# Performance work log

Hardware: AMD Instinct MI355X
Metric: run time of the kernel (lower is better)

## Reference

```python
import jax, jax.numpy as jnp
import numpy as np

B, NQ, DM = 2, 8192, 256
NH, DH, NL, NP = 6, 64, 3, 9
IMG_H, IMG_W = 384, 1280
SHAPES = [(48, 160), (24, 80), (12, 40)]  # (h, w) per pyramid level


def setup_inputs() -> dict:
    key = jax.random.key(0)
    ks = jax.random.split(key, 16)
    inp = {}
    inp["x"] = jax.random.normal(ks[0], (B, NQ, DM), jnp.float32)
    inp["pe"] = jax.random.normal(ks[1], (B, NQ, DM), jnp.float32)
    # lidar points in front of the camera so projected uv mostly lands in-image
    u = jax.random.uniform(ks[2], (B, NQ, 3), jnp.float32)
    inp["coor"] = jnp.stack([(u[..., 0] - 0.5) * 40.0,
                             (u[..., 1] - 0.5) * 4.0,
                             2.0 + u[..., 2] * 48.0], axis=-1)
    K = jnp.array([[700., 0., 640., 0.], [0., 700., 192., 0.],
                   [0., 0., 1., 0.], [0., 0., 0., 1.]], jnp.float32)
    inp["cam2img"] = jnp.broadcast_to(K, (B, 4, 4))
    inp["lidar2cam"] = jnp.broadcast_to(jnp.eye(4, dtype=jnp.float32), (B, 4, 4))
    for i, (h, w) in enumerate(SHAPES):
        inp[f"feat{i}"] = jax.random.normal(ks[3 + i], (B, DM, h, w), jnp.float32) * 0.1
    s = 1.0 / np.sqrt(DM).astype(np.float32)
    inp["W_value"] = jax.random.normal(ks[6], (DM, NH * DH), jnp.float32) * s
    inp["b_value"] = jnp.zeros((NH * DH,), jnp.float32)
    inp["W_off"] = jax.random.normal(ks[7], (DM, NH * NL * NP * 2), jnp.float32) * 0.01
    inp["b_off"] = jax.random.normal(ks[8], (NH * NL * NP * 2,), jnp.float32)
    inp["W_attn"] = jax.random.normal(ks[9], (DM, NH * NL * NP), jnp.float32) * s
    inp["b_attn"] = jnp.zeros((NH * NL * NP,), jnp.float32)
    inp["W_out"] = jax.random.normal(ks[10], (NH * DH, DM), jnp.float32) * (1.0 / np.sqrt(NH * DH)).astype(np.float32)
    inp["b_out"] = jnp.zeros((DM,), jnp.float32)
    return inp


def _points2uv(points, cam2img, lidar2cam):
    R, t = lidar2cam[:, :3, :3], lidar2cam[:, :3, 3]
    pc = jnp.einsum('bij,bnj->bni', R, points) + t[:, None, :]
    Kr, Kt = cam2img[:, :3, :3], cam2img[:, :3, 3]
    p2 = jnp.einsum('bij,bnj->bni', Kr, pc) + Kt[:, None, :]
    return p2[..., :2] / p2[..., 2:3]  # [B,NQ,2] (u,v)


def _bilinear_gather(v, loc, hl, wl):
    # v: [B*NH, hl*wl, DH] values; loc: [B,NQ,NH,NP,2] normalized [0,1]
    # matches grid_sample(bilinear, padding=zeros, align_corners=False)
    x = loc[..., 0] * wl - 0.5
    y = loc[..., 1] * hl - 0.5
    x0 = jnp.floor(x)
    y0 = jnp.floor(y)
    fx = x - x0
    fy = y - y0
    acc = jnp.zeros((B, NH, NQ, NP, DH), v.dtype)
    for dy in (0, 1):
        for dx in (0, 1):
            xi = x0 + dx
            yi = y0 + dy
            wgt = (fx if dx else 1.0 - fx) * (fy if dy else 1.0 - fy)
            valid = (xi >= 0) & (xi < wl) & (yi >= 0) & (yi < hl)
            idx = (jnp.clip(yi, 0, hl - 1) * wl + jnp.clip(xi, 0, wl - 1)).astype(jnp.int32)
            idx = idx.transpose(0, 2, 1, 3).reshape(B * NH, NQ * NP)
            g = jax.vmap(lambda vt, it: vt[it])(v, idx)  # [B*NH, NQ*NP, DH]
            g = g.reshape(B, NH, NQ, NP, DH)
            wv = (wgt * valid).transpose(0, 2, 1, 3)      # [B,NH,NQ,NP]
            acc = acc + g * wv[..., None]
    return acc


def reference(x, pe, coor, cam2img, lidar2cam, feat0, feat1, feat2,
              W_value, b_value, W_off, b_off, W_attn, b_attn, W_out, b_out):
    feats = [feat0, feat1, feat2]
    uv = _points2uv(coor, cam2img, lidar2cam)  # [B,NQ,2]
    # per-level reference points in level pixel coords: uv * (w_l/W, h_l/H)
    ref = jnp.stack([uv * jnp.array([w / IMG_W, h / IMG_H], jnp.float32)
                     for (h, w) in SHAPES], axis=2)  # [B,NQ,NL,2]
    q = x + pe
    off = (q @ W_off + b_off).reshape(B, NQ, NH, NL, NP, 2)
    attn = jax.nn.softmax((q @ W_attn + b_attn).reshape(B, NQ, NH, NL * NP), axis=-1)
    attn = attn.reshape(B, NQ, NH, NL, NP).transpose(0, 2, 1, 3, 4)  # [B,NH,NQ,NL,NP]
    norm = jnp.array([[w, h] for (h, w) in SHAPES], jnp.float32)     # [NL,2] (w,h)
    loc = (ref[:, :, None, :, None, :] + off) / norm[None, None, None, :, None, :]
    out = jnp.zeros((B, NH, NQ, DH), jnp.float32)
    for l, (h, w) in enumerate(SHAPES):
        src = feats[l].reshape(B, DM, h * w).transpose(0, 2, 1)  # [B,hw,DM]
        v = (src @ W_value + b_value).reshape(B, h * w, NH, DH)
        v = v.transpose(0, 2, 1, 3).reshape(B * NH, h * w, DH)
        sampled = _bilinear_gather(v, loc[:, :, :, l], h, w)    # [B,NH,NQ,NP,DH]
        out = out + jnp.einsum('bhqp,bhqpd->bhqd', attn[:, :, :, l], sampled)
    out = out.transpose(0, 2, 1, 3).reshape(B, NQ, NH * DH)
    return out @ W_out + b_out  # dropout is identity at eval
```

## Files before the change

### kernel.cpp

```cpp
#include <hip/hip_runtime.h>
#include <hip/hip_bf16.h>

#define NQ_   8192
#define DM_   256
#define NH_   6
#define DH_   64
#define BATCH 2

typedef __attribute__((ext_vector_type(8))) short short8;
typedef __attribute__((ext_vector_type(4))) short short4v;
typedef __attribute__((ext_vector_type(4))) float float4v;
typedef __attribute__((ext_vector_type(2))) float f32x2;
typedef __attribute__((ext_vector_type(4))) unsigned int uint32x4;
typedef __attribute__((ext_vector_type(4))) int int32x4;

#if defined(__has_builtin)
#if __has_builtin(__builtin_amdgcn_make_buffer_rsrc) && __has_builtin(__builtin_amdgcn_raw_ptr_buffer_load_b128)
#define USE_BUFLD 1
#endif
#endif
#ifndef USE_BUFLD
#define USE_BUFLD 0
#endif

static const size_t VOFF_L0 = 0;
static const size_t VOFF_L1 = 5898240;
static const size_t VOFF_L2 = 7372800;
static const size_t QRAW_BYTE_OFF  = 15482880;
static const size_t MID_BYTE_OFF   = 47333376;
static const size_t QBF_BYTE_OFF   = 47333376;
static const size_t WT_BYTE_OFF    = 59916288;
static const size_t FEATT_BYTE_OFF = 60558336;
static const size_t REF_BYTE_OFF   = 70880256;
static const size_t WVT_OFF   = 0;
static const size_t WOFFT_OFF = 98304;
static const size_t WOUTT_OFF = 222720;
static const size_t FT_L0 = 0;
static const size_t FT_L1 = 3932160;
static const size_t FT_L2 = 4915200;

__device__ __forceinline__ unsigned short f2bf(float f) {
    unsigned int u = __float_as_uint(f);
    unsigned int r = (u + 0x7fffu + ((u >> 16) & 1u)) >> 16;
    return (unsigned short)r;
}

__device__ __forceinline__ void cp16(void* lds, const void* g) {
    __builtin_amdgcn_global_load_lds(
        (const __attribute__((address_space(1))) unsigned int*)g,
        (__attribute__((address_space(3))) unsigned int*)lds, 16, 0, 0);
}

__global__ __launch_bounds__(256) void prep_all(const float* __restrict__ Wv,
                                                const float* __restrict__ Woff,
                                                const float* __restrict__ Wattn,
                                                const float* __restrict__ Wout,
                                                const float* __restrict__ feat0,
                                                const float* __restrict__ feat1,
                                                const float* __restrict__ feat2,
                                                const float* __restrict__ x,
                                                const float* __restrict__ pe,
                                                const float* __restrict__ coor,
                                                const float* __restrict__ cam2img,
                                                const float* __restrict__ l2c,
                                                unsigned short* __restrict__ wT,
                                                unsigned short* __restrict__ fT,
                                                unsigned short* __restrict__ qbf,
                                                float* __restrict__ ref) {
    const int pid = blockIdx.x, t = threadIdx.x;
    if (pid < 1126) {
        int r = pid;
        const float* src; int N, n, K; size_t doff;
        if (r < 384)      { src = Wv;    N = 384; n = r;       K = 256; doff = (size_t)r * 256; }
        else if (r < 708) { src = Woff;  N = 324; n = r - 384; K = 256; doff = (size_t)r * 256; }
        else if (r < 870) { src = Wattn; N = 162; n = r - 708; K = 256; doff = (size_t)r * 256; }
        else              { src = Wout;  N = 256; n = r - 870; K = 384; doff = WOUTT_OFF + (size_t)(r - 870) * 384; }
        for (int k = t; k < K; k += 256) wT[doff + k] = f2bf(src[(size_t)k * N + n]);
        return;
    }
    if (pid < 3646) {
        __shared__ float tile[64][33];
        int f = pid - 1126;
        const float* src; unsigned short* dst; int HW;
        if (f < 1920)      { src = feat0; dst = fT + FT_L0; HW = 7680; }
        else if (f < 2400) { src = feat1; dst = fT + FT_L1; HW = 1920; f -= 1920; }
        else               { src = feat2; dst = fT + FT_L2; HW = 480;  f -= 2400; }
        int pb = f >> 3, rem = f & 7, cb = rem >> 1, b = rem & 1;
        int p0 = pb * 32, c0 = cb * 64;
        {
            int px = t & 31, cy = t >> 5;
#pragma unroll
            for (int i = 0; i < 8; ++i) {
                int cr = cy + i * 8;
                tile[cr][px] = src[((size_t)(b * DM_ + c0 + cr)) * HW + p0 + px];
            }
        }
        __syncthreads();
        {
            int cx = t & 63, py = t >> 6;
#pragma unroll
            for (int i = 0; i < 8; ++i) {
                int pr = py + i * 4;
                dst[((size_t)b * HW + p0 + pr) * DM_ + c0 + cx] = f2bf(tile[cx][pr]);
            }
        }
        return;
    }
    if (pid < 4670) {
        int f = pid - 3646;
#pragma unroll
        for (int i = 0; i < 4; ++i) {
            size_t e = (size_t)f * 4096 + i * 1024 + t * 4;
            float4 xv = *(const float4*)&x[e];
            float4 pv = *(const float4*)&pe[e];
            short4v o;
            o[0] = (short)f2bf(xv.x + pv.x);
            o[1] = (short)f2bf(xv.y + pv.y);
            o[2] = (short)f2bf(xv.z + pv.z);
            o[3] = (short)f2bf(xv.w + pv.w);
            *(short4v*)&qbf[e] = o;
        }
        return;
    }
    {
        int q = (pid - 4670) * 256 + t;
        int b = q >> 13;
        float c0 = coor[(size_t)q * 3 + 0];
        float c1 = coor[(size_t)q * 3 + 1];
        float c2 = coor[(size_t)q * 3 + 2];
        const float* L = l2c + b * 16;
        const float* C = cam2img + b * 16;
        float pc0 = L[0] * c0 + L[1] * c1 + L[2]  * c2 + L[3];
        float pc1 = L[4] * c0 + L[5] * c1 + L[6]  * c2 + L[7];
        float pc2 = L[8] * c0 + L[9] * c1 + L[10] * c2 + L[11];
        float q0 = C[0] * pc0 + C[1] * pc1 + C[2]  * pc2 + C[3];
        float q1 = C[4] * pc0 + C[5] * pc1 + C[6]  * pc2 + C[7];
        float q2 = C[8] * pc0 + C[9] * pc1 + C[10] * pc2 + C[11];
        float rz = __frcp_rn(q2);
        float rx = q0 * rz * 0.125f, ry = q1 * rz * 0.125f;
#pragma unroll
        for (int l = 0; l < 3; ++l) {
            float sl = (l == 0) ? 1.f : ((l == 1) ? 0.5f : 0.25f);
            f32x2 v = {rx * sl - 0.5f, ry * sl - 0.5f};
            *(f32x2*)&ref[(size_t)q * 6 + l * 2] = v;
        }
    }
}

__device__ __forceinline__ void mfma_block32(const short A[][32], const short B[][32],
                                             int wm, int wn, int lane, float4v acc[4][4]) {
    int m_base = wm + (lane & 15);
    int n_base = wn + (lane & 15);
    int q8 = (lane >> 4) * 8;
    short8 af[4], bf[4];
#pragma unroll
    for (int i = 0; i < 4; ++i) af[i] = *(const short8*)&A[m_base + i * 16][q8];
#pragma unroll
    for (int j = 0; j < 4; ++j) bf[j] = *(const short8*)&B[n_base + j * 16][q8];
#pragma unroll
    for (int i = 0; i < 4; ++i)
#pragma unroll
        for (int j = 0; j < 4; ++j)
            acc[i][j] = __builtin_amdgcn_mfma_f32_16x16x32_bf16(af[i], bf[j], acc[i][j], 0, 0, 0);
}

__global__ __launch_bounds__(256) void gemm_vq(const unsigned short* __restrict__ fT,
                                               const unsigned short* __restrict__ wT,
                                               const float* __restrict__ bv,
                                               unsigned short* __restrict__ vws,
                                               const unsigned short* __restrict__ qbf,
                                               const float* __restrict__ boff,
                                               const float* __restrict__ battn,
                                               float* __restrict__ qraw) {
    __shared__ short A[128][32];
    __shared__ short B[128][32];
    const int tid = threadIdx.x;
    const int lane = tid & 63, wave = tid >> 6;
    const int wm = (wave & 1) * 64, wn = (wave >> 1) * 64;
    const int id = blockIdx.x;
    const int r0 = tid >> 2, sg8 = (tid & 3) * 8;
    float4v acc[4][4];
#pragma unroll
    for (int i = 0; i < 4; ++i)
#pragma unroll
        for (int j = 0; j < 4; ++j) acc[i][j] = (float4v){0.f, 0.f, 0.f, 0.f};

    if (id < 474) {
        int pb = id / 6, rem = id % 6;
        int nb = rem >> 1, b = rem & 1;
        int pbl, HW; size_t ftoff, voff;
        if (pb < 60)      { pbl = pb;      HW = 7680; ftoff = FT_L0; voff = VOFF_L0; }
        else if (pb < 75) { pbl = pb - 60; HW = 1920; ftoff = FT_L1; voff = VOFF_L1; }
        else              { pbl = pb - 75; HW = 480;  ftoff = FT_L2; voff = VOFF_L2; }
        const int p0 = pbl * 128, n0 = nb * 128;
        const unsigned short* Asrc = fT + ftoff + (size_t)b * HW * DM_;
        const unsigned short* wvT = wT + WVT_OFF;
        int p1 = p0 + r0;      if (p1 >= HW) p1 = HW - 1;
        int p2 = p0 + r0 + 64; if (p2 >= HW) p2 = HW - 1;

        for (int k0 = 0; k0 < DM_; k0 += 32) {
            cp16(&A[r0][sg8],      &Asrc[(size_t)p1 * DM_ + k0 + sg8]);
            cp16(&A[r0 + 64][sg8], &Asrc[(size_t)p2 * DM_ + k0 + sg8]);
            cp16(&B[r0][sg8],      &wvT[(size_t)(n0 + r0) * DM_ + k0 + sg8]);
            cp16(&B[r0 + 64][sg8], &wvT[(size_t)(n0 + r0 + 64) * DM_ + k0 + sg8]);
            __syncthreads();
            mfma_block32(A, B, wm, wn, lane, acc);
            __syncthreads();
        }
        int colb = n0 + wn + (lane & 15);
        int rowq = (lane >> 4) * 4;
#pragma unroll
        for (int i = 0; i < 4; ++i)
#pragma unroll
            for (int j = 0; j < 4; ++j) {
                int n = colb + j * 16;
                int h = n >> 6, d = n & 63;
                float bias = bv[n];
#pragma unroll
                for (int r = 0; r < 4; ++r) {
                    int p = p0 + wm + i * 16 + rowq + r;
                    if (p < HW)
                        vws[voff + ((size_t)(b * NH_ + h) * HW + p) * DH_ + d] = f2bf(acc[i][j][r] + bias);
                }
            }
    } else {
        int qid = id - 474;
        const int m0 = (qid & 127) * 128, n0 = (qid >> 7) * 128;
        const unsigned short* wq = wT + WOFFT_OFF;

        for (int k0 = 0; k0 < DM_; k0 += 32) {
            cp16(&A[r0][sg8],      &qbf[(size_t)(m0 + r0) * DM_ + k0 + sg8]);
            cp16(&A[r0 + 64][sg8], &qbf[(size_t)(m0 + r0 + 64) * DM_ + k0 + sg8]);
            cp16(&B[r0][sg8],      &wq[(size_t)(n0 + r0) * DM_ + k0 + sg8]);
            cp16(&B[r0 + 64][sg8], &wq[(size_t)(n0 + r0 + 64) * DM_ + k0 + sg8]);
            __syncthreads();
            mfma_block32(A, B, wm, wn, lane, acc);
            __syncthreads();
        }
        int colb = n0 + wn + (lane & 15);
        int rowq = (lane >> 4) * 4;
#pragma unroll
        for (int i = 0; i < 4; ++i)
#pragma unroll
            for (int j = 0; j < 4; ++j) {
                int n = colb + j * 16;
                if (n < 486) {
                    float bias = (n < 324) ? boff[n] : battn[n - 324];
#pragma unroll
                    for (int r = 0; r < 4; ++r) {
                        int m = m0 + wm + i * 16 + rowq + r;
                        qraw[(size_t)m * 486 + n] = acc[i][j][r] + bias;
                    }
                }
            }
    }
}

__global__ __launch_bounds__(384, 5) void sample_kernel(const float* __restrict__ qraw,
                                                        const float* __restrict__ ref,
                                                        const unsigned short* __restrict__ vws,
                                                        unsigned short* __restrict__ mid) {
    __shared__ int2 s_plan[1416];
    const int tid = threadIdx.x;
    const int bq0 = blockIdx.x * 2;

    {
        int q = tid >= 192;
        int t = tid - q * 192;
        int bq = bq0 + q;
        int b = bq >> 13;
        int h = t >> 5, j = t & 31;
        bool act = j < 27;
        float logit = act ? qraw[(size_t)bq * 486 + 324 + h * 27 + j] : -1e30f;
        float m = logit;
#pragma unroll
        for (int msk = 16; msk >= 1; msk >>= 1) m = fmaxf(m, __shfl_xor(m, msk, 32));
        float e = act ? __expf(logit - m) : 0.f;
        float ssum = e;
#pragma unroll
        for (int msk = 16; msk >= 1; msk >>= 1) ssum += __shfl_xor(ssum, msk, 32);
        if (act) {
            float attn = e * __frcp_rn(ssum);
            int l = (j >= 18) ? 2 : ((j >= 9) ? 1 : 0);
            int wl = 160 >> l, hl = 48 >> l;
            int HWl = (l == 0) ? 7680 : ((l == 1) ? 1920 : 480);
            int lvlb = (l == 0) ? 0 : ((l == 1) ? 11796480 : 14745600);
            f32x2 r2 = *(const f32x2*)&ref[(size_t)bq * 6 + l * 2];
            float2 oxy = *(const float2*)&qraw[(size_t)bq * 486 + h * 54 + j * 2];
            float X = r2[0] + oxy.x;
            float Y = r2[1] + oxy.y;
            float x0f = floorf(X), y0f = floorf(Y);
            float fx = X - x0f, fy = Y - y0f;
            int ix = (int)x0f, iy = (int)y0f;
            int bx = min(max(ix, 0), wl - 2);
            float wx0 = ((bx == ix) ? (1.f - fx) : 0.f) + ((bx == ix + 1) ? fx : 0.f);
            float wx1 = ((bx + 1 == ix) ? (1.f - fx) : 0.f) + ((bx + 1 == ix + 1) ? fx : 0.f);
            int cy0 = min(max(iy, 0), hl - 1);
            int cy1 = min(max(iy + 1, 0), hl - 1);
            float wy0 = (iy >= 0 && iy < hl) ? (1.f - fy) : 0.f;
            float wy1 = (iy + 1 >= 0 && iy + 1 < hl) ? fy : 0.f;
            int jj = h * 27 + j;
            int slice = (b * NH_ + h) * HWl;
            int off0 = lvlb + (slice + cy0 * wl + bx) * 128;
            int off1 = lvlb + (slice + cy1 * wl + bx) * 128;
            int pb = q * 4 * 177 + jj;
            s_plan[pb]           = make_int2(off0,       __float_as_int(attn * wy0 * wx0));
            s_plan[pb + 177]     = make_int2(off0 + 128, __float_as_int(attn * wy0 * wx1));
            s_plan[pb + 2 * 177] = make_int2(off1,       __float_as_int(attn * wy1 * wx0));
            s_plan[pb + 3 * 177] = make_int2(off1 + 128, __float_as_int(attn * wy1 * wx1));
        }
    }
    __syncthreads();

    const int h = tid >> 6;
    const int lane = tid & 63;
    const int plane = lane >> 3;
    const unsigned cb = (unsigned)((lane & 7) << 4);
    const int2* pl = &s_plan[plane * 177 + h * 27];
    f32x2 A0 = {0.f, 0.f}, A1 = {0.f, 0.f}, A2 = {0.f, 0.f}, A3 = {0.f, 0.f};

#if USE_BUFLD
    __amdgpu_buffer_rsrc_t vrs = __builtin_amdgcn_make_buffer_rsrc(
        const_cast<unsigned short*>(vws), (short)0, 15482880, 0x00020000);
#else
    const char* vbase = (const char*)vws;
#endif

    int g0 = 0;
#pragma unroll
    for (int g = 0; g < 5; ++g) {
        const int N = (g < 4) ? 6 : 3;
        int2 pw[6];
        uint32x4 d[6];
#pragma unroll
        for (int t = 0; t < N; ++t) pw[t] = pl[g0 + t];
#pragma unroll
        for (int t = 0; t < N; ++t) {
#if USE_BUFLD
            int32x4 t4 = __builtin_amdgcn_raw_ptr_buffer_load_b128(
                vrs, (int)((unsigned)pw[t].x + cb), 0, 0);
            d[t] = __builtin_bit_cast(uint32x4, t4);
#else
            d[t] = *(const uint32x4*)(vbase + ((unsigned)pw[t].x + cb));
#endif
        }
#pragma unroll
        for (int t = 0; t < N; ++t) {
            float w = __int_as_float(pw[t].y);
            f32x2 w2 = {w, w};
            f32x2 v0 = {__uint_as_float(d[t][0] << 16), __uint_as_float(d[t][0] & 0xffff0000u)};
            f32x2 v1 = {__uint_as_float(d[t][1] << 16), __uint_as_float(d[t][1] & 0xffff0000u)};
            f32x2 v2 = {__uint_as_float(d[t][2] << 16), __uint_as_float(d[t][2] & 0xffff0000u)};
            f32x2 v3 = {__uint_as_float(d[t][3] << 16), __uint_as_float(d[t][3] & 0xffff0000u)};
            A0 = __builtin_elementwise_fma(w2, v0, A0);
            A1 = __builtin_elementwise_fma(w2, v1, A1);
            A2 = __builtin_elementwise_fma(w2, v2, A2);
            A3 = __builtin_elementwise_fma(w2, v3, A3);
        }
        g0 += N;
    }

    float a[8] = {A0.x, A0.y, A1.x, A1.y, A2.x, A2.y, A3.x, A3.y};
#pragma unroll
    for (int i = 0; i < 8; ++i) {
        a[i] += __shfl_xor(a[i], 8, 64);
        a[i] += __shfl_xor(a[i], 16, 64);
    }
    if (((lane >> 3) & 3) == 0) {
        int q = lane >> 5;
        uint4 pk;
        pk.x = (unsigned)f2bf(a[0]) | ((unsigned)f2bf(a[1]) << 16);
        pk.y = (unsigned)f2bf(a[2]) | ((unsigned)f2bf(a[3]) << 16);
        pk.z = (unsigned)f2bf(a[4]) | ((unsigned)f2bf(a[5]) << 16);
        pk.w = (unsigned)f2bf(a[6]) | ((unsigned)f2bf(a[7]) << 16);
        *(uint4*)&mid[(size_t)(bq0 + q) * 384 + h * DH_ + ((lane & 7) << 3)] = pk;
    }
}

__global__ __launch_bounds__(256) void out_gemm(const unsigned short* __restrict__ mid,
                                                const unsigned short* __restrict__ woT,
                                                const float* __restrict__ bout,
                                                float* __restrict__ out) {
    __shared__ short A[64][32];
    __shared__ short B[128][32];
    const int tid = threadIdx.x;
    const int m0 = blockIdx.x * 64, n0 = blockIdx.y * 128;
    const int lane = tid & 63, wave = tid >> 6;
    const int wn = wave * 32;
    const int r0 = tid >> 2, sg8 = (tid & 3) * 8;
    float4v acc[4][2];
#pragma unroll
    for (int i = 0; i < 4; ++i)
#pragma unroll
        for (int j = 0; j < 2; ++j) acc[i][j] = (float4v){0.f, 0.f, 0.f, 0.f};

    for (int k0 = 0; k0 < 384; k0 += 32) {
        cp16(&A[r0][sg8],      &mid[(size_t)(m0 + r0) * 384 + k0 + sg8]);
        cp16(&B[r0][sg8],      &woT[(size_t)(n0 + r0) * 384 + k0 + sg8]);
        cp16(&B[r0 + 64][sg8], &woT[(size_t)(n0 + r0 + 64) * 384 + k0 + sg8]);
        __syncthreads();
        {
            int m_base = lane & 15;
            int n_base = wn + (lane & 15);
            int q8 = (lane >> 4) * 8;
            short8 af[4], bf[2];
#pragma unroll
            for (int i = 0; i < 4; ++i) af[i] = *(const short8*)&A[m_base + i * 16][q8];
#pragma unroll
            for (int j = 0; j < 2; ++j) bf[j] = *(const short8*)&B[n_base + j * 16][q8];
#pragma unroll
            for (int i = 0; i < 4; ++i)
#pragma unroll
                for (int j = 0; j < 2; ++j)
                    acc[i][j] = __builtin_amdgcn_mfma_f32_16x16x32_bf16(af[i], bf[j], acc[i][j], 0, 0, 0);
        }
        __syncthreads();
    }
    int colb = n0 + wn + (lane & 15);
    int rowq = (lane >> 4) * 4;
#pragma unroll
    for (int i = 0; i < 4; ++i)
#pragma unroll
        for (int j = 0; j < 2; ++j) {
            int n = colb + j * 16;
            float bias = bout[n];
#pragma unroll
            for (int r = 0; r < 4; ++r) {
                int m = m0 + i * 16 + rowq + r;
                out[(size_t)m * 256 + n] = acc[i][j][r] + bias;
            }
        }
}

extern "C" void kernel_launch(void* const* d_in, const int* in_sizes, int n_in,
                              void* d_out, int out_size, void* d_ws, size_t ws_size,
                              hipStream_t stream) {
    const float* x      = (const float*)d_in[0];
    const float* pe     = (const float*)d_in[1];
    const float* coor   = (const float*)d_in[2];
    const float* c2i    = (const float*)d_in[3];
    const float* l2c    = (const float*)d_in[4];
    const float* feat0  = (const float*)d_in[5];
    const float* feat1  = (const float*)d_in[6];
    const float* feat2  = (const float*)d_in[7];
    const float* Wv     = (const float*)d_in[8];
    const float* bv     = (const float*)d_in[9];
    const float* Woff   = (const float*)d_in[10];
    const float* boff   = (const float*)d_in[11];
    const float* Wattn  = (const float*)d_in[12];
    const float* battn  = (const float*)d_in[13];
    const float* Wout   = (const float*)d_in[14];
    const float* bout   = (const float*)d_in[15];

    unsigned short* vws = (unsigned short*)d_ws;
    float* qraw         = (float*)((char*)d_ws + QRAW_BYTE_OFF);
    unsigned short* mid = (unsigned short*)((char*)d_ws + MID_BYTE_OFF);
    unsigned short* qbf = (unsigned short*)((char*)d_ws + QBF_BYTE_OFF);
    unsigned short* wT  = (unsigned short*)((char*)d_ws + WT_BYTE_OFF);
    unsigned short* fT  = (unsigned short*)((char*)d_ws + FEATT_BYTE_OFF);
    float* ref          = (float*)((char*)d_ws + REF_BYTE_OFF);
    float* out          = (float*)d_out;

    prep_all<<<dim3(4734), 256, 0, stream>>>(Wv, Woff, Wattn, Wout, feat0, feat1, feat2,
                                             x, pe, coor, c2i, l2c, wT, fT, qbf, ref);
    gemm_vq<<<dim3(986), 256, 0, stream>>>(fT, wT, bv, vws, qbf, boff, battn, qraw);
    sample_kernel<<<dim3(BATCH * NQ_ / 2), 384, 0, stream>>>(qraw, ref, vws, mid);
    out_gemm<<<dim3(256, 2), 256, 0, stream>>>(mid, wT + WOUTT_OFF, bout, out);
}
```

Baseline: 213.2 us.

## Compact nonzero-weight sample points per head and use one query per block

The sampling kernel now handles one query per 192-thread block instead of two queries per 384-thread block. During planning it uses a shared atomic counter to drop sampling points whose bilinear weights are all zero (fully outside the feature map). It then pads the remaining points to a multiple of 9 and gathers with a dynamic loop of 9-wide batches. The goal is to skip useless value loads for out-of-bounds points, at the cost of shared atomics, an extra barrier, padding work and a data-dependent trip count. Since most projected points land in-image, the savings may be small.

```diff
diff --git a/kernel.cpp b/kernel.cpp
--- a/kernel.cpp
+++ b/kernel.cpp
@@ -256,20 +256,21 @@
     }
 }
 
-__global__ __launch_bounds__(384, 5) void sample_kernel(const float* __restrict__ qraw,
+__global__ __launch_bounds__(192, 6) void sample_kernel(const float* __restrict__ qraw,
                                                         const float* __restrict__ ref,
                                                         const unsigned short* __restrict__ vws,
                                                         unsigned short* __restrict__ mid) {
-    __shared__ int2 s_plan[1416];
+    __shared__ int2 s_plan[792];
+    __shared__ int s_cnt[6];
     const int tid = threadIdx.x;
-    const int bq0 = blockIdx.x * 2;
+    const int bq = blockIdx.x;
+    const int b = bq >> 13;
+
+    if (tid < 6) s_cnt[tid] = 0;
+    __syncthreads();
 
     {
-        int q = tid >= 192;
-        int t = tid - q * 192;
-        int bq = bq0 + q;
-        int b = bq >> 13;
-        int h = t >> 5, j = t & 31;
+        int h = tid >> 5, j = tid & 31;
         bool act = j < 27;
         float logit = act ? qraw[(size_t)bq * 486 + 324 + h * 27 + j] : -1e30f;
         float m = logit;
@@ -299,24 +300,43 @@
             int cy1 = min(max(iy + 1, 0), hl - 1);
             float wy0 = (iy >= 0 && iy < hl) ? (1.f - fy) : 0.f;
             float wy1 = (iy + 1 >= 0 && iy + 1 < hl) ? fy : 0.f;
-            int jj = h * 27 + j;
-            int slice = (b * NH_ + h) * HWl;
-            int off0 = lvlb + (slice + cy0 * wl + bx) * 128;
-            int off1 = lvlb + (slice + cy1 * wl + bx) * 128;
-            int pb = q * 4 * 177 + jj;
-            s_plan[pb]           = make_int2(off0,       __float_as_int(attn * wy0 * wx0));
-            s_plan[pb + 177]     = make_int2(off0 + 128, __float_as_int(attn * wy0 * wx1));
-            s_plan[pb + 2 * 177] = make_int2(off1,       __float_as_int(attn * wy1 * wx0));
-            s_plan[pb + 3 * 177] = make_int2(off1 + 128, __float_as_int(attn * wy1 * wx1));
+            if ((wy0 + wy1) * (wx0 + wx1) != 0.f) {
+                int slot = atomicAdd(&s_cnt[h], 1);
+                int slice = (b * NH_ + h) * HWl;
+                int off0 = lvlb + (slice + cy0 * wl + bx) * 128;
+                int off1 = lvlb + (slice + cy1 * wl + bx) * 128;
+                s_plan[(0 * 6 + h) * 33 + slot] = make_int2(off0,       __float_as_int(attn * wy0 * wx0));
+                s_plan[(1 * 6 + h) * 33 + slot] = make_int2(off0 + 128, __float_as_int(attn * wy0 * wx1));
+                s_plan[(2 * 6 + h) * 33 + slot] = make_int2(off1,       __float_as_int(attn * wy1 * wx0));
+                s_plan[(3 * 6 + h) * 33 + slot] = make_int2(off1 + 128, __float_as_int(attn * wy1 * wx1));
+            }
         }
     }
     __syncthreads();
 
-    const int h = tid >> 6;
-    const int lane = tid & 63;
-    const int plane = lane >> 3;
-    const unsigned cb = (unsigned)((lane & 7) << 4);
-    const int2* pl = &s_plan[plane * 177 + h * 27];
+    int ntq = 0;
+#pragma unroll
+    for (int h2 = 0; h2 < 6; ++h2) ntq = max(ntq, s_cnt[h2]);
+    ntq = ((ntq + 8) / 9) * 9;
+
+    {
+        int h = tid >> 5, s = tid & 31;
+        int cn = s_cnt[h];
+        if (s >= cn && s < ntq) {
+            int2 z = make_int2(0, 0);
+            s_plan[(0 * 6 + h) * 33 + s] = z;
+            s_plan[(1 * 6 + h) * 33 + s] = z;
+            s_plan[(2 * 6 + h) * 33 + s] = z;
+            s_plan[(3 * 6 + h) * 33 + s] = z;
+        }
+    }
+    __syncthreads();
+
+    const int h = tid >> 5;
+    const int l32 = tid & 31;
+    const int corner = l32 >> 3;
+    const unsigned cb = (unsigned)((l32 & 7) << 4);
+    const int2* pl = &s_plan[(corner * 6 + h) * 33];
     f32x2 A0 = {0.f, 0.f}, A1 = {0.f, 0.f}, A2 = {0.f, 0.f}, A3 = {0.f, 0.f};
 
 #if USE_BUFLD
@@ -326,16 +346,13 @@
     const char* vbase = (const char*)vws;
 #endif
 
-    int g0 = 0;
-#pragma unroll
-    for (int g = 0; g < 5; ++g) {
-        const int N = (g < 4) ? 6 : 3;
-        int2 pw[6];
-        uint32x4 d[6];
-#pragma unroll
-        for (int t = 0; t < N; ++t) pw[t] = pl[g0 + t];
-#pragma unroll
-        for (int t = 0; t < N; ++t) {
+    for (int t0 = 0; t0 < ntq; t0 += 9) {
+        int2 pw[9];
+        uint32x4 d[9];
+#pragma unroll
+        for (int t = 0; t < 9; ++t) pw[t] = pl[t0 + t];
+#pragma unroll
+        for (int t = 0; t < 9; ++t) {
 #if USE_BUFLD
             int32x4 t4 = __builtin_amdgcn_raw_ptr_buffer_load_b128(
                 vrs, (int)((unsigned)pw[t].x + cb), 0, 0);
@@ -345,7 +362,7 @@
 #endif
         }
 #pragma unroll
-        for (int t = 0; t < N; ++t) {
+        for (int t = 0; t < 9; ++t) {
             float w = __int_as_float(pw[t].y);
             f32x2 w2 = {w, w};
             f32x2 v0 = {__uint_as_float(d[t][0] << 16), __uint_as_float(d[t][0] & 0xffff0000u)};
@@ -357,7 +374,6 @@
             A2 = __builtin_elementwise_fma(w2, v2, A2);
             A3 = __builtin_elementwise_fma(w2, v3, A3);
         }
-        g0 += N;
     }
 
     float a[8] = {A0.x, A0.y, A1.x, A1.y, A2.x, A2.y, A3.x, A3.y};
@@ -366,14 +382,13 @@
         a[i] += __shfl_xor(a[i], 8, 64);
         a[i] += __shfl_xor(a[i], 16, 64);
     }
-    if (((lane >> 3) & 3) == 0) {
-        int q = lane >> 5;
+    if (corner == 0) {
         uint4 pk;
         pk.x = (unsigned)f2bf(a[0]) | ((unsigned)f2bf(a[1]) << 16);
         pk.y = (unsigned)f2bf(a[2]) | ((unsigned)f2bf(a[3]) << 16);
         pk.z = (unsigned)f2bf(a[4]) | ((unsigned)f2bf(a[5]) << 16);
         pk.w = (unsigned)f2bf(a[6]) | ((unsigned)f2bf(a[7]) << 16);
-        *(uint4*)&mid[(size_t)(bq0 + q) * 384 + h * DH_ + ((lane & 7) << 3)] = pk;
+        *(uint4*)&mid[(size_t)bq * 384 + h * DH_ + ((l32 & 7) << 3)] = pk;
     }
 }
 
@@ -464,6 +479,6 @@
     prep_all<<<dim3(4734), 256, 0, stream>>>(Wv, Woff, Wattn, Wout, feat0, feat1, feat2,
                                              x, pe, coor, c2i, l2c, wT, fT, qbf, ref);
     gemm_vq<<<dim3(986), 256, 0, stream>>>(fT, wT, bv, vws, qbf, boff, battn, qraw);
-    sample_kernel<<<dim3(BATCH * NQ_ / 2), 384, 0, stream>>>(qraw, ref, vws, mid);
+    sample_kernel<<<dim3(BATCH * NQ_), 192, 0, stream>>>(qraw, ref, vws, mid);
     out_gemm<<<dim3(256, 2), 256, 0, stream>>>(mid, wT + WOUTT_OFF, bout, out);
 }
```

Measured after the change: 207.4 us. 2.7% less time.
